# Optimization experiments

Measured on AMD Instinct MI355X. Metric: run time of the kernel, lower is better.

The kernel has to match this reference:

```python
import jax, jax.numpy as jnp
import numpy as np

SAMPLE_RATE = 24000.0
SIGMA_MULT = 4.0
CHUNK = 512  # atoms processed per scan step (mirrors chunked Triton kernel)


def setup_inputs() -> dict:
    key = jax.random.key(0)
    ks = jax.random.split(key, 6)
    N = 4096
    num_samples = 72000  # 3 seconds at 24kHz
    duration = num_samples / SAMPLE_RATE
    amplitude = 0.1 * jax.random.normal(ks[0], (N,), dtype=jnp.float32)
    tau = jax.random.uniform(ks[1], (N,), dtype=jnp.float32) * duration
    omega = jax.random.uniform(ks[2], (N,), dtype=jnp.float32) * 8000.0
    sigma = 0.002 + jax.random.uniform(ks[3], (N,), dtype=jnp.float32) * 0.020
    phi = jax.random.uniform(ks[4], (N,), dtype=jnp.float32) * (2.0 * np.pi)
    gamma = 500.0 * jax.random.normal(ks[5], (N,), dtype=jnp.float32)
    return {"amplitude": amplitude, "tau": tau, "omega": omega,
            "sigma": sigma, "phi": phi, "gamma": gamma,
            "num_samples": num_samples}


def _render(amplitude, tau, omega, sigma, phi, gamma, num_samples):
    t = jnp.arange(num_samples, dtype=jnp.float32) / SAMPLE_RATE  # [T]
    two_pi = jnp.float32(2.0 * np.pi)

    def chunk_sum(acc, params):
        a, tu, om, sg, ph, gm = params  # each [CHUNK]
        tc = t[None, :] - tu[:, None]                    # [C,T]
        mask = jnp.abs(tc) <= SIGMA_MULT * sg[:, None]
        env = jnp.exp(-tc * tc / (2.0 * sg[:, None] ** 2 + 1e-8))
        phase = two_pi * (om[:, None] * tc + 0.5 * gm[:, None] * tc * tc) + ph[:, None]
        atoms = a[:, None] * env * jnp.cos(phase) * mask.astype(jnp.float32)
        return acc + atoms.sum(axis=0), None

    N = amplitude.shape[0]
    rs = lambda x: x.reshape(N // CHUNK, CHUNK)
    params = (rs(amplitude), rs(tau), rs(omega), rs(sigma), rs(phi), rs(gamma))
    out, _ = jax.lax.scan(chunk_sum, jnp.zeros((num_samples,), jnp.float32), params)
    return out


def reference(amplitude, tau, omega, sigma, phi, gamma, num_samples):
    return _render(amplitude, tau, omega, sigma, phi, gamma, num_samples)
```

## Files before the change

### kernel.cpp

```cpp
#include <hip/hip_runtime.h>
#include <math.h>


#define SR         24000.0f
#define TWO_PI     6.2831853071795864769f
#define LOG2E      1.4426950408889634f

#define TS     512
#define RBLOCK 128
#define SPT    4
#define SEGS   8
#define MAXA   512

__global__ __launch_bounds__(64) void prep_kernel(
        const float* __restrict__ tau,
        const float* __restrict__ sigma,
        int*   __restrict__ counts,
        int*   __restrict__ lists,
        float* __restrict__ out,
        int N, int T, int ntiles) {
    const int b    = blockIdx.x;
    const int lane = threadIdx.x;

    if (b < ntiles) {
        const float tstart = (float)(b * TS) * (1.0f / SR);
        const float tend   = (float)(b * TS + TS - 1) * (1.0f / SR);
        const float slack  = 2.0f / SR;
        int cnt = 0;
        for (int c = 0; c < N; c += 64) {
            const int ai = c + lane;
            bool hit = false;
            if (ai < N) {
                const float tu = tau[ai];
                const float w  = 4.0f * sigma[ai] + slack;
                hit = ((tu - w) <= tend) && ((tu + w) >= tstart);
            }
            const unsigned long long m = __ballot(hit);
            if (hit) {
                const int pos = cnt + (int)__popcll(m & ((1ull << lane) - 1ull));
                if (pos < MAXA) lists[b * MAXA + pos] = ai;
            }
            cnt += (int)__popcll(m);
        }
        if (lane == 0) counts[b] = (cnt < MAXA) ? cnt : MAXA;
    } else {
        const int i4 = (b - ntiles) * 64 + lane;
        if (i4 * 4 < T) ((float4*)out)[i4] = make_float4(0.f, 0.f, 0.f, 0.f);
    }
}

__global__ __launch_bounds__(RBLOCK) void render_kernel(
        const float* __restrict__ amp,
        const float* __restrict__ tau,
        const float* __restrict__ omega,
        const float* __restrict__ sigma,
        const float* __restrict__ phi,
        const float* __restrict__ gamma,
        const int*   __restrict__ counts,
        const int*   __restrict__ lists,
        float*       __restrict__ out,
        int T) {
    __shared__ float4 s_par[RBLOCK][2];

    const int tile = blockIdx.x;
    const int seg  = blockIdx.y;
    const int tid  = threadIdx.x;
    const int s_base = tile * TS;
    const float t0 = (float)(s_base + tid) * (1.0f / SR);
    const float dt = (float)RBLOCK * (1.0f / SR);

    int cnt = counts[tile];
    const int per = (cnt + SEGS - 1) / SEGS;
    const int a0 = seg * per;
    const int a1 = min(cnt, a0 + per);

    const int* lst = lists + tile * MAXA;
    float acc[SPT] = {0.0f, 0.0f, 0.0f, 0.0f};

    for (int base = a0; base < a1; base += RBLOCK) {
        const int m = min(RBLOCK, a1 - base);
        __syncthreads();
        if (tid < m) {
            const int idx = lst[base + tid];
            const float a  = amp[idx];
            const float tu = tau[idx];
            const float om = omega[idx];
            const float sg = sigma[idx];
            const float ph = phi[idx];
            const float gm = gamma[idx];
            const float k  = -LOG2E / (2.0f * sg * sg + 1e-8f);
            s_par[tid][0] = make_float4(a, tu, om, 0.5f * gm);
            s_par[tid][1] = make_float4(k, ph * (1.0f / TWO_PI), 0.0f, 0.0f);
        }
        __syncthreads();

        for (int i = 0; i < m; ++i) {
            const float4 p0 = s_par[i][0];
            const float4 p1 = s_par[i][1];
            const float tc0 = t0 - p0.y;
            #pragma unroll
            for (int j = 0; j < SPT; ++j) {
                const float tc  = tc0 + (float)j * dt;
                const float tc2 = tc * tc;
                const float env = exp2f(p1.x * tc2);
                const float rev = fmaf(p0.z, tc, fmaf(p0.w, tc2, p1.y));
                const float r   = rev - floorf(rev);
                const float c   = __builtin_amdgcn_cosf(r);
                acc[j] = fmaf(p0.x * env, c, acc[j]);
            }
        }
    }

    #pragma unroll
    for (int j = 0; j < SPT; ++j) {
        const int t_idx = s_base + tid + j * RBLOCK;
        if (t_idx < T && a1 > a0) atomicAdd(&out[t_idx], acc[j]);
    }
}

extern "C" void kernel_launch(void* const* d_in, const int* in_sizes, int n_in,
                              void* d_out, int out_size, void* d_ws, size_t ws_size,
                              hipStream_t stream) {
    const float* amp   = (const float*)d_in[0];
    const float* tau   = (const float*)d_in[1];
    const float* omega = (const float*)d_in[2];
    const float* sigma = (const float*)d_in[3];
    const float* phi   = (const float*)d_in[4];
    const float* gamma = (const float*)d_in[5];

    float* out = (float*)d_out;
    const int T = out_size;
    const int N = in_sizes[0];
    const int ntiles = (T + TS - 1) / TS;

    char* ws = (char*)d_ws;
    int* counts = (int*)ws;
    int* lists  = (int*)(ws + (size_t)ntiles * sizeof(int));

    const int zblocks = (T / 4 + 63) / 64;
    prep_kernel<<<ntiles + zblocks, 64, 0, stream>>>(tau, sigma, counts, lists,
                                                     out, N, T, ntiles);
    dim3 grid(ntiles, SEGS);
    render_kernel<<<grid, RBLOCK, 0, stream>>>(amp, tau, omega, sigma, phi, gamma,
                                               counts, lists, out, T);
}
```

Baseline: 95.34 us.

## Use single-wavefront render blocks with shuffle-broadcast atom params and batch prep loads

The render kernel now runs one 64-lane wavefront per block, with 32 segments per tile and 8 samples per lane. Each lane loads one atom's parameters into registers, and the loop broadcasts them with __shfl, which removes the shared-memory staging and __syncthreads. Segments with no atoms now return early. The prep kernel issues four 64-atom batches of tau/sigma loads before doing the ballots, to hide memory latency in its serial scan over N. The trade-off is four times as many atomicAdds per output sample, and it relies on each segment holding at most 64 atoms, which holds because MAXA/SEGS = 16.

```diff
diff --git a/kernel.cpp b/kernel.cpp
--- a/kernel.cpp
+++ b/kernel.cpp
@@ -7,9 +7,8 @@
 #define LOG2E      1.4426950408889634f
 
 #define TS     512
-#define RBLOCK 128
-#define SPT    4
-#define SEGS   8
+#define SPT    8
+#define SEGS   32
 #define MAXA   512
 
 __global__ __launch_bounds__(64) void prep_kernel(
@@ -27,20 +26,24 @@
         const float tend   = (float)(b * TS + TS - 1) * (1.0f / SR);
         const float slack  = 2.0f / SR;
         int cnt = 0;
-        for (int c = 0; c < N; c += 64) {
-            const int ai = c + lane;
-            bool hit = false;
-            if (ai < N) {
-                const float tu = tau[ai];
-                const float w  = 4.0f * sigma[ai] + slack;
-                hit = ((tu - w) <= tend) && ((tu + w) >= tstart);
+        for (int c = 0; c < N; c += 256) {
+            float tu[4], w[4];
+            #pragma unroll
+            for (int u = 0; u < 4; ++u) {
+                const int ai = c + u * 64 + lane;
+                tu[u] = (ai < N) ? tau[ai]   : 1e9f;
+                w[u]  = (ai < N) ? (4.0f * sigma[ai] + slack) : 0.0f;
             }
-            const unsigned long long m = __ballot(hit);
-            if (hit) {
-                const int pos = cnt + (int)__popcll(m & ((1ull << lane) - 1ull));
-                if (pos < MAXA) lists[b * MAXA + pos] = ai;
+            #pragma unroll
+            for (int u = 0; u < 4; ++u) {
+                const bool hit = ((tu[u] - w[u]) <= tend) && ((tu[u] + w[u]) >= tstart);
+                const unsigned long long mb = __ballot(hit);
+                if (hit) {
+                    const int pos = cnt + (int)__popcll(mb & ((1ull << lane) - 1ull));
+                    if (pos < MAXA) lists[b * MAXA + pos] = c + u * 64 + lane;
+                }
+                cnt += (int)__popcll(mb);
             }
-            cnt += (int)__popcll(m);
         }
         if (lane == 0) counts[b] = (cnt < MAXA) ? cnt : MAXA;
     } else {
@@ -49,7 +52,7 @@
     }
 }
 
-__global__ __launch_bounds__(RBLOCK) void render_kernel(
+__global__ __launch_bounds__(64) void render_kernel(
         const float* __restrict__ amp,
         const float* __restrict__ tau,
         const float* __restrict__ omega,
@@ -60,61 +63,59 @@
         const int*   __restrict__ lists,
         float*       __restrict__ out,
         int T) {
-    __shared__ float4 s_par[RBLOCK][2];
-
     const int tile = blockIdx.x;
     const int seg  = blockIdx.y;
-    const int tid  = threadIdx.x;
-    const int s_base = tile * TS;
-    const float t0 = (float)(s_base + tid) * (1.0f / SR);
-    const float dt = (float)RBLOCK * (1.0f / SR);
+    const int lane = threadIdx.x;
 
-    int cnt = counts[tile];
+    const int cnt = counts[tile];
     const int per = (cnt + SEGS - 1) / SEGS;
-    const int a0 = seg * per;
-    const int a1 = min(cnt, a0 + per);
+    const int a0  = seg * per;
+    const int a1  = min(cnt, a0 + per);
+    const int m   = a1 - a0;
+    if (m <= 0) return;
 
-    const int* lst = lists + tile * MAXA;
-    float acc[SPT] = {0.0f, 0.0f, 0.0f, 0.0f};
+    float pa = 0.f, ptu = 0.f, pom = 0.f, phg = 0.f, pk = 0.f, pph = 0.f;
+    if (lane < m) {
+        const int idx = lists[tile * MAXA + a0 + lane];
+        pa  = amp[idx];
+        ptu = tau[idx];
+        pom = omega[idx];
+        phg = 0.5f * gamma[idx];
+        pph = phi[idx] * (1.0f / TWO_PI);
+        const float sg = sigma[idx];
+        pk  = -LOG2E / (2.0f * sg * sg + 1e-8f);
+    }
 
-    for (int base = a0; base < a1; base += RBLOCK) {
-        const int m = min(RBLOCK, a1 - base);
-        __syncthreads();
-        if (tid < m) {
-            const int idx = lst[base + tid];
-            const float a  = amp[idx];
-            const float tu = tau[idx];
-            const float om = omega[idx];
-            const float sg = sigma[idx];
-            const float ph = phi[idx];
-            const float gm = gamma[idx];
-            const float k  = -LOG2E / (2.0f * sg * sg + 1e-8f);
-            s_par[tid][0] = make_float4(a, tu, om, 0.5f * gm);
-            s_par[tid][1] = make_float4(k, ph * (1.0f / TWO_PI), 0.0f, 0.0f);
-        }
-        __syncthreads();
+    const int   s_base = tile * TS;
+    const float t0 = (float)(s_base + lane) * (1.0f / SR);
+    const float dt = 64.0f * (1.0f / SR);
 
-        for (int i = 0; i < m; ++i) {
-            const float4 p0 = s_par[i][0];
-            const float4 p1 = s_par[i][1];
-            const float tc0 = t0 - p0.y;
-            #pragma unroll
-            for (int j = 0; j < SPT; ++j) {
-                const float tc  = tc0 + (float)j * dt;
-                const float tc2 = tc * tc;
-                const float env = exp2f(p1.x * tc2);
-                const float rev = fmaf(p0.z, tc, fmaf(p0.w, tc2, p1.y));
-                const float r   = rev - floorf(rev);
-                const float c   = __builtin_amdgcn_cosf(r);
-                acc[j] = fmaf(p0.x * env, c, acc[j]);
-            }
+    float acc[SPT] = {0.f, 0.f, 0.f, 0.f, 0.f, 0.f, 0.f, 0.f};
+
+    for (int i = 0; i < m; ++i) {
+        const float ai_ = __shfl(pa,  i);
+        const float tui = __shfl(ptu, i);
+        const float omi = __shfl(pom, i);
+        const float hgi = __shfl(phg, i);
+        const float ki  = __shfl(pk,  i);
+        const float phi_= __shfl(pph, i);
+        const float tc0 = t0 - tui;
+        #pragma unroll
+        for (int j = 0; j < SPT; ++j) {
+            const float tc  = tc0 + (float)j * dt;
+            const float tc2 = tc * tc;
+            const float env = exp2f(ki * tc2);
+            const float rev = fmaf(omi, tc, fmaf(hgi, tc2, phi_));
+            const float r   = rev - floorf(rev);
+            const float c   = __builtin_amdgcn_cosf(r);
+            acc[j] = fmaf(ai_ * env, c, acc[j]);
         }
     }
 
     #pragma unroll
     for (int j = 0; j < SPT; ++j) {
-        const int t_idx = s_base + tid + j * RBLOCK;
-        if (t_idx < T && a1 > a0) atomicAdd(&out[t_idx], acc[j]);
+        const int t_idx = s_base + lane + j * 64;
+        if (t_idx < T) atomicAdd(&out[t_idx], acc[j]);
     }
 }
 
@@ -141,6 +142,6 @@
     prep_kernel<<<ntiles + zblocks, 64, 0, stream>>>(tau, sigma, counts, lists,
                                                      out, N, T, ntiles);
     dim3 grid(ntiles, SEGS);
-    render_kernel<<<grid, RBLOCK, 0, stream>>>(amp, tau, omega, sigma, phi, gamma,
-                                               counts, lists, out, T);
+    render_kernel<<<grid, 64, 0, stream>>>(amp, tau, omega, sigma, phi, gamma,
+                                           counts, lists, out, T);
 }
```

New measurement: 95.44 us. Within noise of the previous version (+0.1%).
